# Kernel tuning notes

Measured on AMD Instinct MI355X. Metric: run time of the kernel, lower is better.

## Reference

```python
import jax, jax.numpy as jnp
import numpy as np

D_MODEL = 1024
NUM_HEAD = 16
D_K = D_MODEL // NUM_HEAD
FFN_D = 4096
EPS = 1e-5


def _layernorm(x, gamma, beta):
    mu = jnp.mean(x, axis=-1, keepdims=True)
    var = jnp.mean(jnp.square(x - mu), axis=-1, keepdims=True)
    return (x - mu) * jax.lax.rsqrt(var + EPS) * gamma + beta


def setup_inputs() -> dict:
    key = jax.random.key(0)
    ks = jax.random.split(key, 16)
    s = 1.0 / np.sqrt(D_MODEL)
    sf = 1.0 / np.sqrt(FFN_D)
    # weights stored as [in, out] (transpose of torch nn.Linear.weight)
    return {
        "x": jax.random.normal(ks[0], (4, 2048, D_MODEL), dtype=jnp.float32),
        "wq": jax.random.uniform(ks[1], (D_MODEL, D_MODEL), jnp.float32, -s, s),
        "bq": jax.random.uniform(ks[2], (D_MODEL,), jnp.float32, -s, s),
        "wk": jax.random.uniform(ks[3], (D_MODEL, D_MODEL), jnp.float32, -s, s),
        "bk": jax.random.uniform(ks[4], (D_MODEL,), jnp.float32, -s, s),
        "wv": jax.random.uniform(ks[5], (D_MODEL, D_MODEL), jnp.float32, -s, s),
        "bv": jax.random.uniform(ks[6], (D_MODEL,), jnp.float32, -s, s),
        "wo": jax.random.uniform(ks[7], (D_MODEL, D_MODEL), jnp.float32, -s, s),
        "bo": jax.random.uniform(ks[8], (D_MODEL,), jnp.float32, -s, s),
        "w1": jax.random.uniform(ks[9], (D_MODEL, FFN_D), jnp.float32, -s, s),
        "b1": jax.random.uniform(ks[10], (FFN_D,), jnp.float32, -s, s),
        "w2": jax.random.uniform(ks[11], (FFN_D, D_MODEL), jnp.float32, -sf, sf),
        "b2": jax.random.uniform(ks[12], (D_MODEL,), jnp.float32, -sf, sf),
        "g1": jnp.ones((D_MODEL,), jnp.float32),
        "be1": jnp.zeros((D_MODEL,), jnp.float32),
        "g2": jnp.ones((D_MODEL,), jnp.float32),
        "be2": jnp.zeros((D_MODEL,), jnp.float32),
    }


def reference(x, wq, bq, wk, bk, wv, bv, wo, bo, w1, b1, w2, b2, g1, be1, g2, be2):
    B, S, _ = x.shape
    resid1 = x
    # project and split heads: [B, H, S, d_k]
    def heads(w, b):
        return (x @ w + b).reshape(B, S, NUM_HEAD, D_K).transpose(0, 2, 1, 3)
    q = heads(wq, bq)
    k = heads(wk, bk)
    v = heads(wv, bv)
    scores = jnp.einsum("bhsd,bhtd->bhst", q, k) / jnp.sqrt(jnp.float32(D_K))
    attn = jax.nn.softmax(scores, axis=-1)
    ctx = jnp.einsum("bhst,bhtd->bhsd", attn, v)
    ctx = ctx.transpose(0, 2, 1, 3).reshape(B, S, D_MODEL)
    attn_out = ctx @ wo + bo
    x1 = _layernorm(resid1 + attn_out, g1, be1)
    ffn = jax.nn.relu(x1 @ w1 + b1) @ w2 + b2
    return _layernorm(x1 + ffn, g2, be2)
```

## Files before the change

kernel.cpp:

```cpp
#include <hip/hip_runtime.h>

typedef unsigned short u16;
typedef __attribute__((ext_vector_type(8))) u16 u16x8;
typedef __attribute__((ext_vector_type(8))) __bf16 bf16x8;
typedef __attribute__((ext_vector_type(4))) float floatx4;
typedef __attribute__((ext_vector_type(16))) float floatx16;
typedef __attribute__((ext_vector_type(4))) unsigned int u32x4;

#define MFMA16(a, b, c) __builtin_amdgcn_mfma_f32_16x16x32_bf16( \
    __builtin_bit_cast(bf16x8, a), __builtin_bit_cast(bf16x8, b), c, 0, 0, 0)
#define MFMA32(a, b, c) __builtin_amdgcn_mfma_f32_32x32x16_bf16( \
    __builtin_bit_cast(bf16x8, a), __builtin_bit_cast(bf16x8, b), c, 0, 0, 0)

#if __has_builtin(__builtin_amdgcn_exp2f)
#define EXP2(x) __builtin_amdgcn_exp2f(x)
#else
#define EXP2(x) exp2f(x)
#endif

__device__ __forceinline__ float bf2f(u16 h) {
  unsigned u = ((unsigned)h) << 16;
  float f;
  __builtin_memcpy(&f, &u, 4);
  return f;
}
__device__ __forceinline__ u16 f2bf(float f) {
  unsigned u;
  __builtin_memcpy(&u, &f, 4);
  u += 0x7fff + ((u >> 16) & 1);
  return (u16)(u >> 16);
}

__device__ __forceinline__ unsigned cvt_pk_bf16(float a, float b) {
  unsigned r;
  asm("v_cvt_pk_bf16_f32 %0, %1, %2" : "=v"(r) : "v"(a), "v"(b));
  return r;
}
__device__ __forceinline__ void pl32_swap(unsigned& a, unsigned& b) {
  asm("v_permlane32_swap_b32 %0, %1" : "+v"(a), "+v"(b));
}

typedef __attribute__((address_space(1))) const unsigned int gas_u32;
typedef __attribute__((address_space(3))) unsigned int las_u32;

__device__ __forceinline__ void gld_lds16(const u16* g, u16* l) {
  __builtin_amdgcn_global_load_lds((gas_u32*)g, (las_u32*)l, 16, 0, 0);
}

__global__ __launch_bounds__(256) void transpose_k(const float* __restrict__ in,
                                                   u16* __restrict__ out, int R, int C) {
  __shared__ u16 tile[64][65];
  int c0 = blockIdx.x * 64, r0 = blockIdx.y * 64;
  int tc = threadIdx.x & 63, tr = threadIdx.x >> 6;
#pragma unroll
  for (int i = 0; i < 16; ++i)
    tile[tr + i * 4][tc] = f2bf(in[(size_t)(r0 + tr + i * 4) * C + c0 + tc]);
  __syncthreads();
#pragma unroll
  for (int i = 0; i < 16; ++i)
    out[(size_t)(c0 + tr + i * 4) * R + r0 + tc] = tile[tc][tr + i * 4];
}

__global__ __launch_bounds__(256) void transpose4_k(const float* __restrict__ i0,
                                                    const float* __restrict__ i1,
                                                    const float* __restrict__ i2,
                                                    const float* __restrict__ i3,
                                                    u16* __restrict__ o0, u16* __restrict__ o1,
                                                    u16* __restrict__ o2, u16* __restrict__ o3) {
  __shared__ u16 tile[64][65];
  const float* in;
  u16* out;
  switch (blockIdx.z) {
    case 0: in = i0; out = o0; break;
    case 1: in = i1; out = o1; break;
    case 2: in = i2; out = o2; break;
    default: in = i3; out = o3; break;
  }
  int c0 = blockIdx.x * 64, r0 = blockIdx.y * 64;
  int tc = threadIdx.x & 63, tr = threadIdx.x >> 6;
#pragma unroll
  for (int i = 0; i < 16; ++i)
    tile[tr + i * 4][tc] = f2bf(in[(size_t)(r0 + tr + i * 4) * 1024 + c0 + tc]);
  __syncthreads();
#pragma unroll
  for (int i = 0; i < 16; ++i)
    out[(size_t)(c0 + tr + i * 4) * 1024 + r0 + tc] = tile[tc][tr + i * 4];
}

__global__ __launch_bounds__(256) void convert_k(const float* __restrict__ in,
                                                 u16* __restrict__ out) {
  size_t idx = ((size_t)blockIdx.x * 256 + threadIdx.x) * 8;
  floatx4 f0 = *(const floatx4*)(in + idx);
  floatx4 f1 = *(const floatx4*)(in + idx + 4);
  u16x8 o;
#pragma unroll
  for (int e = 0; e < 4; ++e) o[e] = f2bf(f0[e]);
#pragma unroll
  for (int e = 0; e < 4; ++e) o[4 + e] = f2bf(f1[e]);
  *(u16x8*)(out + idx) = o;
}

template <bool C_F32, bool BIAS_ROW>
__global__ __launch_bounds__(256, 2) void gemm_bt(const u16* __restrict__ A,
                                                  const u16* __restrict__ BT,
                                                  const float* __restrict__ bias,
                                                  const float* __restrict__ bias2, int bsplit,
                                                  void* __restrict__ Cv, int M, int N, int K,
                                                  int relu) {
  __shared__ __align__(16) u16 As[2][128 * 64];
  __shared__ __align__(16) u16 Bs[2][128 * 64];
  const int tid = threadIdx.x, lane = tid & 63, wave = tid >> 6;
  const int quad = lane >> 4, l15 = lane & 15;
  const int wr = wave >> 1, wc = wave & 1;
  const int m0 = blockIdx.x * 128, n0 = blockIdx.y * 128;

  floatx4 acc[4][4] = {};

  auto stage = [&](int kt, int buf) {
    int k0 = kt * 64;
#pragma unroll
    for (int p = 0; p < 4; ++p) {
      int chunk = p * 256 + tid;
      int row = chunk >> 3, cc = chunk & 7;
      int gc = cc ^ (row & 7);
      int ldsoff = (p * 256 + wave * 64) * 8;
      gld_lds16(A + (size_t)(m0 + row) * K + k0 + gc * 8, &As[buf][ldsoff]);
      gld_lds16(BT + (size_t)(n0 + row) * K + k0 + gc * 8, &Bs[buf][ldsoff]);
    }
  };

  const int nk = K >> 6;
  stage(0, 0);

  for (int kt = 0; kt < nk; ++kt) {
    const int cur = kt & 1;
    __syncthreads();
    if (kt + 1 < nk) stage(kt + 1, cur ^ 1);

#pragma unroll
    for (int ks = 0; ks < 2; ++ks) {
      u16x8 af[4], bfr[4];
#pragma unroll
      for (int i = 0; i < 4; ++i) {
        int r = wr * 64 + i * 16 + l15;
        af[i] = *(const u16x8*)(&As[cur][r * 64 + (((ks * 4 + quad) ^ (r & 7)) * 8)]);
      }
#pragma unroll
      for (int j = 0; j < 4; ++j) {
        int r = wc * 64 + j * 16 + l15;
        bfr[j] = *(const u16x8*)(&Bs[cur][r * 64 + (((ks * 4 + quad) ^ (r & 7)) * 8)]);
      }
#pragma unroll
      for (int i = 0; i < 4; ++i)
#pragma unroll
        for (int j = 0; j < 4; ++j) acc[i][j] = MFMA16(af[i], bfr[j], acc[i][j]);
    }
  }

#pragma unroll
  for (int j = 0; j < 4; ++j) {
    int col = n0 + wc * 64 + j * 16 + l15;
    float bv = 0.f;
    if (!BIAS_ROW) bv = col < bsplit ? bias[col] : bias2[col - bsplit];
#pragma unroll
    for (int i = 0; i < 4; ++i) {
      int row = m0 + wr * 64 + i * 16 + quad * 4;
#pragma unroll
      for (int r = 0; r < 4; ++r) {
        float v = acc[i][j][r] + (BIAS_ROW ? bias[row + r] : bv);
        if (relu) v = fmaxf(v, 0.f);
        if (C_F32)
          ((float*)Cv)[(size_t)(row + r) * N + col] = v;
        else
          ((u16*)Cv)[(size_t)(row + r) * N + col] = f2bf(v);
      }
    }
  }
}

__global__ __launch_bounds__(1024, 4) void gemm256_k(const u16* __restrict__ A,
                                                     const u16* __restrict__ BT,
                                                     const float* __restrict__ bias,
                                                     const float* __restrict__ bias2,
                                                     int bsplit, u16* __restrict__ C, int M,
                                                     int N, int K, int relu) {
  __shared__ __align__(16) u16 As[2][256 * 64];
  __shared__ __align__(16) u16 Bs[2][256 * 64];
  const int tid = threadIdx.x, lane = tid & 63, wave = tid >> 6;
  const int quad = lane >> 4, l15 = lane & 15;
  const int wm = wave >> 2, wn = wave & 3;
  const int m0 = blockIdx.x * 256, n0 = blockIdx.y * 256;

  floatx4 acc[4][4] = {};

  auto stage = [&](int kt, int buf) {
    int k0 = kt * 64;
#pragma unroll
    for (int p = 0; p < 2; ++p) {
      int chunk = p * 1024 + tid;
      int row = chunk >> 3, cc = chunk & 7;
      int gc = cc ^ (row & 7);
      int ldsoff = (p * 1024 + wave * 64) * 8;
      gld_lds16(A + (size_t)(m0 + row) * K + k0 + gc * 8, &As[buf][ldsoff]);
      gld_lds16(BT + (size_t)(n0 + row) * K + k0 + gc * 8, &Bs[buf][ldsoff]);
    }
  };

  const int nk = K >> 6;
  stage(0, 0);

  for (int kt = 0; kt < nk; ++kt) {
    const int cur = kt & 1;
    __syncthreads();
    if (kt + 1 < nk) stage(kt + 1, cur ^ 1);

#pragma unroll
    for (int ks = 0; ks < 2; ++ks) {
      u16x8 af[4], bfr[4];
#pragma unroll
      for (int i = 0; i < 4; ++i) {
        int r = wm * 64 + i * 16 + l15;
        af[i] = *(const u16x8*)(&As[cur][r * 64 + (((ks * 4 + quad) ^ (r & 7)) * 8)]);
      }
#pragma unroll
      for (int j = 0; j < 4; ++j) {
        int r = wn * 64 + j * 16 + l15;
        bfr[j] = *(const u16x8*)(&Bs[cur][r * 64 + (((ks * 4 + quad) ^ (r & 7)) * 8)]);
      }
#pragma unroll
      for (int i = 0; i < 4; ++i)
#pragma unroll
        for (int j = 0; j < 4; ++j) acc[i][j] = MFMA16(af[i], bfr[j], acc[i][j]);
    }
  }

#pragma unroll
  for (int j = 0; j < 4; ++j) {
    int col = n0 + wn * 64 + j * 16 + l15;
    float bv = col < bsplit ? bias[col] : bias2[col - bsplit];
#pragma unroll
    for (int i = 0; i < 4; ++i) {
      int row = m0 + wm * 64 + i * 16 + quad * 4;
#pragma unroll
      for (int r = 0; r < 4; ++r) {
        float v = acc[i][j][r] + bv;
        if (relu) v = fmaxf(v, 0.f);
        C[(size_t)(row + r) * N + col] = f2bf(v);
      }
    }
  }
}

__global__ __launch_bounds__(256, 4) void attn_k(const u16* __restrict__ Q,
                                                 const u16* __restrict__ Km,
                                                 const u16* __restrict__ Vt,
                                                 u16* __restrict__ O) {
  __shared__ __align__(16) u16 sh[16384];
  const int tid = threadIdx.x, lane = tid & 63, w = tid >> 6;
  const int hi = lane >> 5, l31 = lane & 31;
  const int b = blockIdx.z, h = blockIdx.y, q0 = blockIdx.x * 128;
  const size_t tokbase = (size_t)b * 2048;

#pragma unroll
  for (int p = 0; p < 4; ++p) {
    int chunk = p * 256 + tid, row = chunk >> 3, cc = chunk & 7;
    int gc = cc ^ (row & 7);
    gld_lds16(Q + (tokbase + q0 + row) * 2048 + h * 64 + gc * 8, sh + (p * 256 + w * 64) * 8);
  }
  __syncthreads();
  u16x8 qf[4];
#pragma unroll
  for (int kt = 0; kt < 4; ++kt) {
    int r = w * 32 + l31;
    int sel = (kt * 2 + hi) ^ (r & 7);
    u16x8 t = *(const u16x8*)(sh + r * 64 + sel * 8);
#pragma unroll
    for (int e = 0; e < 8; ++e) t[e] = f2bf(bf2f(t[e]) * 0.18033688011f);
    qf[kt] = t;
  }
  __syncthreads();

  floatx16 oacc0 = {}, oacc1 = {};
  float lsum = 0.f;

  auto stage = [&](int it2, int buf) {
    int t0 = it2 * 64;
#pragma unroll
    for (int p = 0; p < 2; ++p) {
      int chunk = p * 256 + tid;
      int row = chunk >> 3, cc = chunk & 7;
      int gc = cc ^ (row & 7);
      int ldsoff = (p * 256 + w * 64) * 8;
      gld_lds16(Km + (tokbase + t0 + row) * 2048 + h * 64 + gc * 8, sh + buf * 4096 + ldsoff);
      gld_lds16(Vt + ((size_t)(h * 64 + row)) * 8192 + tokbase + t0 + gc * 8,
                sh + 8192 + buf * 4096 + ldsoff);
    }
  };

  stage(0, 0);

  for (int it = 0; it < 32; ++it) {
    const int cur = it & 1;
    __syncthreads();
    if (it + 1 < 32) stage(it + 1, cur ^ 1);
    const u16* kb = sh + cur * 4096;
    const u16* vb = sh + 8192 + cur * 4096;

    u32x4 pf[4];
#pragma unroll
    for (int tt = 0; tt < 2; ++tt) {
      u16x8 ka[4];
#pragma unroll
      for (int kt = 0; kt < 4; ++kt) {
        int r = tt * 32 + l31;
        ka[kt] = *(const u16x8*)(kb + r * 64 + (((kt * 2 + hi) ^ (r & 7)) * 8));
      }
      floatx16 s = {};
      __builtin_amdgcn_s_setprio(1);
#pragma unroll
      for (int kt = 0; kt < 4; ++kt) s = MFMA32(ka[kt], qf[kt], s);
      __builtin_amdgcn_s_setprio(0);

      float p[16];
#pragma unroll
      for (int r = 0; r < 16; ++r) p[r] = EXP2(s[r]);
#pragma unroll
      for (int r = 0; r < 16; ++r) lsum += p[r];
#pragma unroll
      for (int half = 0; half < 2; ++half) {
        unsigned X0 = cvt_pk_bf16(p[half * 8 + 0], p[half * 8 + 1]);
        unsigned X1 = cvt_pk_bf16(p[half * 8 + 2], p[half * 8 + 3]);
        unsigned Y0 = cvt_pk_bf16(p[half * 8 + 4], p[half * 8 + 5]);
        unsigned Y1 = cvt_pk_bf16(p[half * 8 + 6], p[half * 8 + 7]);
        pl32_swap(X0, Y0);
        pl32_swap(X1, Y1);
        u32x4 f;
        f[0] = X0; f[1] = X1; f[2] = Y0; f[3] = Y1;
        pf[tt * 2 + half] = f;
      }
    }

    {
      u16x8 va[4];
#pragma unroll
      for (int kt = 0; kt < 4; ++kt) {
        int r = l31;
        va[kt] = *(const u16x8*)(vb + r * 64 + (((kt * 2 + hi) ^ (r & 7)) * 8));
      }
      __builtin_amdgcn_s_setprio(1);
#pragma unroll
      for (int kt = 0; kt < 4; ++kt)
        oacc0 = MFMA32(va[kt], __builtin_bit_cast(u16x8, pf[kt]), oacc0);
      __builtin_amdgcn_s_setprio(0);
#pragma unroll
      for (int kt = 0; kt < 4; ++kt) {
        int r = 32 + l31;
        va[kt] = *(const u16x8*)(vb + r * 64 + (((kt * 2 + hi) ^ (r & 7)) * 8));
      }
      __builtin_amdgcn_s_setprio(1);
#pragma unroll
      for (int kt = 0; kt < 4; ++kt)
        oacc1 = MFMA32(va[kt], __builtin_bit_cast(u16x8, pf[kt]), oacc1);
      __builtin_amdgcn_s_setprio(0);
    }
  }

  __syncthreads();
  float tot = lsum + __shfl_xor(lsum, 32);
  float inv = 1.0f / fmaxf(tot, 1e-30f);
  const int qrow = w * 32 + l31;
#pragma unroll
  for (int dt = 0; dt < 2; ++dt) {
    const floatx16& oa = dt ? oacc1 : oacc0;
#pragma unroll
    for (int pr = 0; pr < 8; ++pr) {
      float a = oa[2 * pr] * inv, bb = oa[2 * pr + 1] * inv;
      unsigned pkw = (unsigned)f2bf(a) | ((unsigned)f2bf(bb) << 16);
      int d = dt * 32 + (pr & 1) * 2 + (pr >> 1) * 8 + 4 * hi;
      *(unsigned*)(sh + qrow * 72 + d) = pkw;
    }
  }
  __syncthreads();
#pragma unroll
  for (int p2 = 0; p2 < 4; ++p2) {
    int c = p2 * 64 + lane, rl = c >> 3, cc = c & 7;
    u16x8 vv = *(const u16x8*)(sh + (w * 32 + rl) * 72 + cc * 8);
    *(u16x8*)(O + (tokbase + q0 + w * 32 + rl) * 1024 + h * 64 + cc * 8) = vv;
  }
}

template <bool A_F32, bool B_F32, bool OUT_F32>
__global__ __launch_bounds__(256) void ln_k(const void* __restrict__ Av,
                                            const void* __restrict__ Bv,
                                            const float* __restrict__ g,
                                            const float* __restrict__ be,
                                            void* __restrict__ outv) {
  const int lane = threadIdx.x & 63, wave = threadIdx.x >> 6;
  const size_t row = (size_t)blockIdx.x * 4 + wave;
  const size_t base = row * 1024 + lane * 16;
  float v[16];
  if (A_F32) {
    const float* a = (const float*)Av + base;
#pragma unroll
    for (int q = 0; q < 4; ++q) {
      floatx4 t = *(const floatx4*)(a + q * 4);
#pragma unroll
      for (int e = 0; e < 4; ++e) v[q * 4 + e] = t[e];
    }
  } else {
    const u16* a = (const u16*)Av + base;
    u16x8 a0 = *(const u16x8*)a, a1 = *(const u16x8*)(a + 8);
#pragma unroll
    for (int e = 0; e < 8; ++e) {
      v[e] = bf2f(a0[e]);
      v[e + 8] = bf2f(a1[e]);
    }
  }
  if (B_F32) {
    const float* bb = (const float*)Bv + base;
#pragma unroll
    for (int q = 0; q < 4; ++q) {
      floatx4 t = *(const floatx4*)(bb + q * 4);
#pragma unroll
      for (int e = 0; e < 4; ++e) v[q * 4 + e] += t[e];
    }
  } else {
    const u16* bb = (const u16*)Bv + base;
    u16x8 b0 = *(const u16x8*)bb, b1 = *(const u16x8*)(bb + 8);
#pragma unroll
    for (int e = 0; e < 8; ++e) {
      v[e] += bf2f(b0[e]);
      v[e + 8] += bf2f(b1[e]);
    }
  }
  float sum = 0.f, sq = 0.f;
#pragma unroll
  for (int e = 0; e < 16; ++e) {
    sum += v[e];
    sq += v[e] * v[e];
  }
#pragma unroll
  for (int mk = 1; mk < 64; mk <<= 1) {
    sum += __shfl_xor(sum, mk);
    sq += __shfl_xor(sq, mk);
  }
  float mu = sum * (1.f / 1024.f);
  float var = fmaxf(sq * (1.f / 1024.f) - mu * mu, 0.f);
  float rstd = rsqrtf(var + 1e-5f);
  if (OUT_F32) {
    float* o = (float*)outv + base;
#pragma unroll
    for (int q = 0; q < 4; ++q) {
      floatx4 t;
#pragma unroll
      for (int e = 0; e < 4; ++e) {
        int c = lane * 16 + q * 4 + e;
        t[e] = (v[q * 4 + e] - mu) * rstd * g[c] + be[c];
      }
      *(floatx4*)(o + q * 4) = t;
    }
  } else {
    u16x8 o0, o1;
#pragma unroll
    for (int e = 0; e < 8; ++e) {
      int c = lane * 16 + e;
      o0[e] = f2bf((v[e] - mu) * rstd * g[c] + be[c]);
      o1[e] = f2bf((v[e + 8] - mu) * rstd * g[c + 8] + be[c + 8]);
    }
    *(u16x8*)((u16*)outv + base) = o0;
    *(u16x8*)((u16*)outv + base + 8) = o1;
  }
}

extern "C" void kernel_launch(void* const* d_in, const int* in_sizes, int n_in, void* d_out,
                              int out_size, void* d_ws, size_t ws_size, hipStream_t stream) {
  const float* x = (const float*)d_in[0];
  const float* wq = (const float*)d_in[1];
  const float* bq = (const float*)d_in[2];
  const float* wk = (const float*)d_in[3];
  const float* bk = (const float*)d_in[4];
  const float* wv = (const float*)d_in[5];
  const float* bv = (const float*)d_in[6];
  const float* wo = (const float*)d_in[7];
  const float* bo = (const float*)d_in[8];
  const float* w1 = (const float*)d_in[9];
  const float* b1 = (const float*)d_in[10];
  const float* w2 = (const float*)d_in[11];
  const float* b2 = (const float*)d_in[12];
  const float* g1 = (const float*)d_in[13];
  const float* be1 = (const float*)d_in[14];
  const float* g2 = (const float*)d_in[15];
  const float* be2 = (const float*)d_in[16];
  float* out = (float*)d_out;

  u16* W = (u16*)d_ws;
  const size_t M1 = (size_t)1 << 20;
  u16* wqT = W;
  u16* wkT = wqT + M1;
  u16* wvT = wkT + M1;
  u16* woT = wvT + M1;
  u16* w1T = woT + M1;
  u16* w2T = w1T + 4 * M1;
  u16* arena = w2T + 4 * M1;
  const size_t S8M = (size_t)8 << 20;
  u16* xb = arena;
  u16* QKb = arena + S8M;
  u16* Vtb = arena + 3 * S8M;
  u16* Cb = arena + 4 * S8M;
  u16* AO = arena + 5 * S8M;
  u16* X1 = xb;
  u16* F1 = QKb;
  const int NOSPLIT = 1 << 30;

  dim3 blk(256);
  transpose4_k<<<dim3(16, 16, 4), blk, 0, stream>>>(wq, wk, wv, wo, wqT, wkT, wvT, woT);
  transpose_k<<<dim3(64, 16), blk, 0, stream>>>(w1, w1T, 1024, 4096);
  transpose_k<<<dim3(16, 64), blk, 0, stream>>>(w2, w2T, 4096, 1024);
  convert_k<<<4096, blk, 0, stream>>>(x, xb);

  gemm256_k<<<dim3(32, 8), dim3(1024), 0, stream>>>(xb, wqT, bq, bk, 1024, QKb, 8192, 2048,
                                                    1024, 0);
  gemm_bt<false, true><<<dim3(8, 64), blk, 0, stream>>>(wvT, xb, bv, bv, NOSPLIT, Vtb, 1024,
                                                        8192, 1024, 0);

  attn_k<<<dim3(16, 16, 4), blk, 0, stream>>>(QKb, QKb + 1024, Vtb, Cb);

  gemm_bt<false, false><<<dim3(64, 8), blk, 0, stream>>>(Cb, woT, bo, bo, NOSPLIT, AO, 8192,
                                                         1024, 1024, 0);
  ln_k<true, false, false><<<2048, blk, 0, stream>>>(x, AO, g1, be1, X1);

  gemm256_k<<<dim3(32, 16), dim3(1024), 0, stream>>>(X1, w1T, b1, b1, NOSPLIT, F1, 8192, 4096,
                                                     1024, 1);
  gemm_bt<true, false><<<dim3(64, 8), blk, 0, stream>>>(F1, w2T, b2, b2, NOSPLIT, out, 8192,
                                                        1024, 4096, 0);
  ln_k<false, true, true><<<2048, blk, 0, stream>>>(X1, out, g2, be2, out);
}
```

Measured before the change: 495.4 us.

## Merge prep kernels, fuse QK and V-transpose GEMMs, drop 256-tile GEMM

Folds the four weight-transpose and input-convert launches into a single prep kernel that dispatches on block index. The QK projection and the transposed V projection now run in one launch on 128x128 tiles, and the FFN1 GEMM switches from the 256x256, 1024-thread kernel to the generic 128x128 gemm_bt. The aim is to cut launch overhead and tail idle time between small kernels, and to fill the GPU with one larger grid. In exchange, the smaller tiles give less operand reuse per block for the QK and FFN1 GEMMs.

```diff
diff --git a/kernel.cpp b/kernel.cpp
--- a/kernel.cpp
+++ b/kernel.cpp
@@ -47,57 +47,58 @@
   __builtin_amdgcn_global_load_lds((gas_u32*)g, (las_u32*)l, 16, 0, 0);
 }
 
-__global__ __launch_bounds__(256) void transpose_k(const float* __restrict__ in,
-                                                   u16* __restrict__ out, int R, int C) {
+__global__ __launch_bounds__(256) void prep_k(
+    const float* __restrict__ wq, const float* __restrict__ wk,
+    const float* __restrict__ wv, const float* __restrict__ wo, u16* __restrict__ wqT,
+    u16* __restrict__ wkT, u16* __restrict__ wvT, u16* __restrict__ woT,
+    const float* __restrict__ w1, const float* __restrict__ w2, u16* __restrict__ w1T,
+    u16* __restrict__ w2T, const float* __restrict__ x, u16* __restrict__ xb) {
   __shared__ u16 tile[64][65];
-  int c0 = blockIdx.x * 64, r0 = blockIdx.y * 64;
-  int tc = threadIdx.x & 63, tr = threadIdx.x >> 6;
-#pragma unroll
-  for (int i = 0; i < 16; ++i)
-    tile[tr + i * 4][tc] = f2bf(in[(size_t)(r0 + tr + i * 4) * C + c0 + tc]);
-  __syncthreads();
-#pragma unroll
-  for (int i = 0; i < 16; ++i)
-    out[(size_t)(c0 + tr + i * 4) * R + r0 + tc] = tile[tc][tr + i * 4];
-}
-
-__global__ __launch_bounds__(256) void transpose4_k(const float* __restrict__ i0,
-                                                    const float* __restrict__ i1,
-                                                    const float* __restrict__ i2,
-                                                    const float* __restrict__ i3,
-                                                    u16* __restrict__ o0, u16* __restrict__ o1,
-                                                    u16* __restrict__ o2, u16* __restrict__ o3) {
-  __shared__ u16 tile[64][65];
-  const float* in;
-  u16* out;
-  switch (blockIdx.z) {
-    case 0: in = i0; out = o0; break;
-    case 1: in = i1; out = o1; break;
-    case 2: in = i2; out = o2; break;
-    default: in = i3; out = o3; break;
-  }
-  int c0 = blockIdx.x * 64, r0 = blockIdx.y * 64;
-  int tc = threadIdx.x & 63, tr = threadIdx.x >> 6;
-#pragma unroll
-  for (int i = 0; i < 16; ++i)
-    tile[tr + i * 4][tc] = f2bf(in[(size_t)(r0 + tr + i * 4) * 1024 + c0 + tc]);
-  __syncthreads();
-#pragma unroll
-  for (int i = 0; i < 16; ++i)
-    out[(size_t)(c0 + tr + i * 4) * 1024 + r0 + tc] = tile[tc][tr + i * 4];
-}
-
-__global__ __launch_bounds__(256) void convert_k(const float* __restrict__ in,
-                                                 u16* __restrict__ out) {
-  size_t idx = ((size_t)blockIdx.x * 256 + threadIdx.x) * 8;
-  floatx4 f0 = *(const floatx4*)(in + idx);
-  floatx4 f1 = *(const floatx4*)(in + idx + 4);
-  u16x8 o;
-#pragma unroll
-  for (int e = 0; e < 4; ++e) o[e] = f2bf(f0[e]);
-#pragma unroll
-  for (int e = 0; e < 4; ++e) o[4 + e] = f2bf(f1[e]);
-  *(u16x8*)(out + idx) = o;
+  const int id = blockIdx.x;
+  if (id < 3072) {
+    const float* in;
+    u16* out;
+    int R, C, r0, c0;
+    if (id < 1024) {
+      int bx = id & 15, by = (id >> 4) & 15, bz = id >> 8;
+      switch (bz) {
+        case 0: in = wq; out = wqT; break;
+        case 1: in = wk; out = wkT; break;
+        case 2: in = wv; out = wvT; break;
+        default: in = wo; out = woT; break;
+      }
+      R = 1024; C = 1024;
+      c0 = bx * 64; r0 = by * 64;
+    } else {
+      int l = id - 1024;
+      int bx = l & 63, by = (l >> 6) & 15, bz = l >> 10;
+      if (bz == 0) {
+        in = w1; out = w1T; R = 1024; C = 4096;
+        c0 = bx * 64; r0 = by * 64;
+      } else {
+        in = w2; out = w2T; R = 4096; C = 1024;
+        r0 = bx * 64; c0 = by * 64;
+      }
+    }
+    int tc = threadIdx.x & 63, tr = threadIdx.x >> 6;
+#pragma unroll
+    for (int i = 0; i < 16; ++i)
+      tile[tr + i * 4][tc] = f2bf(in[(size_t)(r0 + tr + i * 4) * C + c0 + tc]);
+    __syncthreads();
+#pragma unroll
+    for (int i = 0; i < 16; ++i)
+      out[(size_t)(c0 + tr + i * 4) * R + r0 + tc] = tile[tc][tr + i * 4];
+  } else {
+    size_t idx = ((size_t)(id - 3072) * 256 + threadIdx.x) * 8;
+    floatx4 f0 = *(const floatx4*)(x + idx);
+    floatx4 f1 = *(const floatx4*)(x + idx + 4);
+    u16x8 o;
+#pragma unroll
+    for (int e = 0; e < 4; ++e) o[e] = f2bf(f0[e]);
+#pragma unroll
+    for (int e = 0; e < 4; ++e) o[4 + e] = f2bf(f1[e]);
+    *(u16x8*)(xb + idx) = o;
+  }
 }
 
 template <bool C_F32, bool BIAS_ROW>
@@ -178,29 +179,42 @@
   }
 }
 
-__global__ __launch_bounds__(1024, 4) void gemm256_k(const u16* __restrict__ A,
-                                                     const u16* __restrict__ BT,
-                                                     const float* __restrict__ bias,
-                                                     const float* __restrict__ bias2,
-                                                     int bsplit, u16* __restrict__ C, int M,
-                                                     int N, int K, int relu) {
-  __shared__ __align__(16) u16 As[2][256 * 64];
-  __shared__ __align__(16) u16 Bs[2][256 * 64];
+__global__ __launch_bounds__(256, 2) void gemm_qkvt_k(
+    const u16* __restrict__ xb, const u16* __restrict__ wqkT, const float* __restrict__ bq,
+    const float* __restrict__ bk, u16* __restrict__ QKb, const u16* __restrict__ wvT,
+    const float* __restrict__ bv, u16* __restrict__ Vtb) {
+  __shared__ __align__(16) u16 As[2][128 * 64];
+  __shared__ __align__(16) u16 Bs[2][128 * 64];
   const int tid = threadIdx.x, lane = tid & 63, wave = tid >> 6;
   const int quad = lane >> 4, l15 = lane & 15;
-  const int wm = wave >> 2, wn = wave & 3;
-  const int m0 = blockIdx.x * 256, n0 = blockIdx.y * 256;
+  const int wr = wave >> 1, wc = wave & 1;
+
+  const u16 *A, *BT;
+  u16* C;
+  const float *bias, *bias2;
+  int N, m0, n0, bsplit, rowbias;
+  if (blockIdx.y < 16) {
+    A = xb; BT = wqkT; C = QKb; bias = bq; bias2 = bk;
+    bsplit = 1024; rowbias = 0; N = 2048;
+    m0 = blockIdx.x * 128; n0 = blockIdx.y * 128;
+  } else {
+    int l = blockIdx.x + (blockIdx.y - 16) * 64;
+    A = wvT; BT = xb; C = Vtb; bias = bv; bias2 = bv;
+    bsplit = 1 << 30; rowbias = 1; N = 8192;
+    m0 = (l & 7) * 128; n0 = (l >> 3) * 128;
+  }
+  const int K = 1024;
 
   floatx4 acc[4][4] = {};
 
   auto stage = [&](int kt, int buf) {
     int k0 = kt * 64;
 #pragma unroll
-    for (int p = 0; p < 2; ++p) {
-      int chunk = p * 1024 + tid;
+    for (int p = 0; p < 4; ++p) {
+      int chunk = p * 256 + tid;
       int row = chunk >> 3, cc = chunk & 7;
       int gc = cc ^ (row & 7);
-      int ldsoff = (p * 1024 + wave * 64) * 8;
+      int ldsoff = (p * 256 + wave * 64) * 8;
       gld_lds16(A + (size_t)(m0 + row) * K + k0 + gc * 8, &As[buf][ldsoff]);
       gld_lds16(BT + (size_t)(n0 + row) * K + k0 + gc * 8, &Bs[buf][ldsoff]);
     }
@@ -219,12 +233,12 @@
       u16x8 af[4], bfr[4];
 #pragma unroll
       for (int i = 0; i < 4; ++i) {
-        int r = wm * 64 + i * 16 + l15;
+        int r = wr * 64 + i * 16 + l15;
         af[i] = *(const u16x8*)(&As[cur][r * 64 + (((ks * 4 + quad) ^ (r & 7)) * 8)]);
       }
 #pragma unroll
       for (int j = 0; j < 4; ++j) {
-        int r = wn * 64 + j * 16 + l15;
+        int r = wc * 64 + j * 16 + l15;
         bfr[j] = *(const u16x8*)(&Bs[cur][r * 64 + (((ks * 4 + quad) ^ (r & 7)) * 8)]);
       }
 #pragma unroll
@@ -236,15 +250,15 @@
 
 #pragma unroll
   for (int j = 0; j < 4; ++j) {
-    int col = n0 + wn * 64 + j * 16 + l15;
-    float bv = col < bsplit ? bias[col] : bias2[col - bsplit];
+    int col = n0 + wc * 64 + j * 16 + l15;
+    float bv2 = 0.f;
+    if (!rowbias) bv2 = col < bsplit ? bias[col] : bias2[col - bsplit];
 #pragma unroll
     for (int i = 0; i < 4; ++i) {
-      int row = m0 + wm * 64 + i * 16 + quad * 4;
+      int row = m0 + wr * 64 + i * 16 + quad * 4;
 #pragma unroll
       for (int r = 0; r < 4; ++r) {
-        float v = acc[i][j][r] + bv;
-        if (relu) v = fmaxf(v, 0.f);
+        float v = acc[i][j][r] + (rowbias ? bias[row + r] : bv2);
         C[(size_t)(row + r) * N + col] = f2bf(v);
       }
     }
@@ -513,15 +527,10 @@
   const int NOSPLIT = 1 << 30;
 
   dim3 blk(256);
-  transpose4_k<<<dim3(16, 16, 4), blk, 0, stream>>>(wq, wk, wv, wo, wqT, wkT, wvT, woT);
-  transpose_k<<<dim3(64, 16), blk, 0, stream>>>(w1, w1T, 1024, 4096);
-  transpose_k<<<dim3(16, 64), blk, 0, stream>>>(w2, w2T, 4096, 1024);
-  convert_k<<<4096, blk, 0, stream>>>(x, xb);
-
-  gemm256_k<<<dim3(32, 8), dim3(1024), 0, stream>>>(xb, wqT, bq, bk, 1024, QKb, 8192, 2048,
-                                                    1024, 0);
-  gemm_bt<false, true><<<dim3(8, 64), blk, 0, stream>>>(wvT, xb, bv, bv, NOSPLIT, Vtb, 1024,
-                                                        8192, 1024, 0);
+  prep_k<<<7168, blk, 0, stream>>>(wq, wk, wv, wo, wqT, wkT, wvT, woT, w1, w2, w1T, w2T, x,
+                                   xb);
+
+  gemm_qkvt_k<<<dim3(64, 24), blk, 0, stream>>>(xb, wqT, bq, bk, QKb, wvT, bv, Vtb);
 
   attn_k<<<dim3(16, 16, 4), blk, 0, stream>>>(QKb, QKb + 1024, Vtb, Cb);
 
@@ -529,8 +538,8 @@
                                                          1024, 1024, 0);
   ln_k<true, false, false><<<2048, blk, 0, stream>>>(x, AO, g1, be1, X1);
 
-  gemm256_k<<<dim3(32, 16), dim3(1024), 0, stream>>>(X1, w1T, b1, b1, NOSPLIT, F1, 8192, 4096,
-                                                     1024, 1);
+  gemm_bt<false, false><<<dim3(64, 32), blk, 0, stream>>>(X1, w1T, b1, b1, NOSPLIT, F1, 8192,
+                                                          4096, 1024, 1);
   gemm_bt<true, false><<<dim3(64, 8), blk, 0, stream>>>(F1, w2T, b2, b2, NOSPLIT, out, 8192,
                                                         1024, 4096, 0);
   ln_k<false, true, true><<<2048, blk, 0, stream>>>(X1, out, g2, be2, out);
```

Result: slower. 516.5 us (+4.3%).
